# Performance work log

Measured on AMD Instinct MI355X. Metric: run time of the kernel, lower is better.

## Reference

```python
import jax, jax.numpy as jnp
import numpy as np

WS = 7       # window_size
NH = 4       # num_head = dim_in // dim_head
HD = 64      # dim_head
ALPHA = 0.1
BETA = 0.2
THETA = 0.5
EPS = 1e-5   # LayerNorm eps


def dwconv(x, w):
    # x: [b, C, h, w], w: [C, 1, k, k] depthwise, padding 'same', no bias
    return jax.lax.conv_general_dilated(
        x, w, window_strides=(1, 1), padding='SAME',
        feature_group_count=x.shape[1],
        dimension_numbers=('NCHW', 'OIHW', 'NCHW'))


def setup_inputs() -> dict:
    key = jax.random.key(0)
    ks = jax.random.split(key, 8)
    B, H, W, C = 32, 56, 56, 256
    s = 0.02
    return {
        'x': jax.random.normal(ks[0], (B, H, W, C), jnp.float32),
        'qkv_w': jax.random.normal(ks[1], (3 * C, C), jnp.float32) * s,
        'qkv_b': jnp.zeros((3 * C,), jnp.float32),
        'conv3_w': jax.random.normal(ks[2], (C, 1, 3, 3), jnp.float32) * s,
        'conv5_w': jax.random.normal(ks[3], (C, 1, 5, 5), jnp.float32) * s,
        'conv7_w': jax.random.normal(ks[4], (C, 1, 7, 7), jnp.float32) * s,
        'ffn_in_w': jax.random.normal(ks[5], (C, C), jnp.float32) * s,
        'ffn_out_w': jax.random.normal(ks[6], (C, C), jnp.float32) * s,
        'ln_g': jnp.ones((C,), jnp.float32),
        'ln_b': jnp.zeros((C,), jnp.float32),
    }


def reference(x, qkv_w, qkv_b, conv3_w, conv5_w, conv7_w, ffn_in_w, ffn_out_w, ln_g, ln_b):
    B, H, W, C = x.shape
    n1, n2 = H // WS, W // WS  # H,W divisible by WS -> no padding path
    # rearrange 'b (h1 n1) (w1 n2) c -> (b n1 n2) h1 w1 c' (window dim is MAJOR axis)
    xw = x.reshape(B, WS, n1, WS, n2, C).transpose(0, 2, 4, 1, 3, 5)
    xw = xw.reshape(B * n1 * n2, WS, WS, C)
    b, hw = B * n1 * n2, WS * WS

    shortcut = xw.reshape(b, hw, NH, HD).transpose(0, 2, 1, 3)  # [b, nh, hw, hd]
    qkv = xw.reshape(b, hw, C) @ qkv_w.T + qkv_b                # [b, hw, 3C]
    qkv = qkv.reshape(b, hw, 3, NH, HD).transpose(2, 0, 3, 1, 4)
    q, k, v = qkv[0], qkv[1], qkv[2]
    v = ALPHA * v + shortcut                                     # scaled residual into V
    shortcut2 = v.transpose(0, 2, 1, 3).reshape(b, WS, WS, C)    # [b, h, w, C]

    # SDPA with default scale hd^-0.5
    attn = jax.nn.softmax(jnp.einsum('bnqd,bnkd->bnqk', q, k) * (HD ** -0.5), axis=-1)
    x_spa = jnp.einsum('bnqk,bnkd->bnqd', attn, v)
    x_spa = x_spa.transpose(0, 2, 1, 3).reshape(b, WS, WS, C)

    # conv branches on modified v: v.transpose(-1,-2).reshape(b, C, h, w)
    xc = v.transpose(0, 1, 3, 2).reshape(b, C, WS, WS)
    c3 = dwconv(xc, conv3_w).transpose(0, 2, 3, 1)
    c5 = dwconv(xc, conv5_w).transpose(0, 2, 3, 1)
    c7 = dwconv(xc, conv7_w).transpose(0, 2, 3, 1)
    x_spa = 0.25 * (x_spa + c3 + c5 + c7)  # equal 0.25 branch weights

    xw = BETA * x_spa + shortcut2
    # inverse rearrange '(b n1 n2) h1 w1 c -> b (h1 n1) (w1 n2) c'
    xo = xw.reshape(B, n1, n2, WS, WS, C).transpose(0, 3, 1, 4, 2, 5).reshape(B, H, W, C)

    # FFN (bias=False) with scaled residual, then LayerNorm
    y = jax.nn.silu(xo @ ffn_in_w.T) @ ffn_out_w.T
    xo = THETA * y + xo
    mu = jnp.mean(xo, axis=-1, keepdims=True)
    var = jnp.var(xo, axis=-1, keepdims=True)
    return (xo - mu) / jnp.sqrt(var + EPS) * ln_g + ln_b
```

## Files before the change

kernel.cpp:

```cpp
#include <hip/hip_runtime.h>

typedef unsigned short u16;
typedef unsigned short u16x8 __attribute__((ext_vector_type(8)));
typedef unsigned short u16x4 __attribute__((ext_vector_type(4)));
typedef unsigned int   u32x2 __attribute__((ext_vector_type(2)));
typedef short          s16x8 __attribute__((ext_vector_type(8)));
typedef float          f32x4 __attribute__((ext_vector_type(4)));

#define DEV static __device__ __forceinline__

DEV float bf2f(u16 u){ unsigned int v = ((unsigned int)u) << 16; return __builtin_bit_cast(float, v); }
DEV u16 f2bf(float f){
  unsigned int u = __builtin_bit_cast(unsigned int, f);
  u += 0x7fffu + ((u >> 16) & 1u);
  return (u16)(u >> 16);
}

DEV f32x4 mfma16(u16x8 a, u16x8 b, f32x4 c){
  return __builtin_amdgcn_mfma_f32_16x16x32_bf16(
      __builtin_bit_cast(s16x8, a), __builtin_bit_cast(s16x8, b), c, 0, 0, 0);
}

DEV void g2l16(const void* g, void* l){
  __builtin_amdgcn_global_load_lds((const __attribute__((address_space(1))) void*)g,
                                   (__attribute__((address_space(3))) void*)l, 16, 0, 0);
}

DEV size_t xrow_from(int b, int hw){
  int h1 = hw / 7, w1 = hw - h1 * 7;
  return ((size_t)(((b >> 6) * 56 + h1 * 8 + ((b >> 3) & 7)) * 56 + (w1 * 8 + (b & 7)))) << 8;
}
DEV size_t xrow_off(int t){ int b = t / 49; return xrow_from(b, t - b * 49); }

__global__ __launch_bounds__(256) void k_prep(const float* __restrict__ qkvw,
                                              const float* __restrict__ c3,
                                              const float* __restrict__ c5,
                                              const float* __restrict__ c7,
                                              const float* __restrict__ fin,
                                              const float* __restrict__ fout,
                                              u16* __restrict__ wq, u16* __restrict__ wfi,
                                              u16* __restrict__ wfo, float* __restrict__ weff){
  int id = blockIdx.x * 256 + threadIdx.x;
  if (id < 196608) { wq[id] = f2bf(qkvw[id]); return; }
  id -= 196608;
  if (id < 65536) { wfi[id] = f2bf(fin[id]); return; }
  id -= 65536;
  if (id < 65536) { wfo[id] = f2bf(fout[id]); return; }
  id -= 65536;
  if (id < 12544) {
    int c = id / 49, t = id - c * 49;
    int di = t / 7 - 3, dj = t % 7 - 3;
    float s = c7[c * 49 + t];
    if (di >= -2 && di <= 2 && dj >= -2 && dj <= 2) s += c5[c * 25 + (di + 2) * 5 + (dj + 2)];
    if (di >= -1 && di <= 1 && dj >= -1 && dj <= 1) s += c3[c * 9 + (di + 1) * 3 + (dj + 1)];
    weff[t * 256 + c] = 0.05f * s;
  }
}

__global__ __launch_bounds__(256) void k_xbf(const float* __restrict__ x, u16* __restrict__ xbf){
  int tid = threadIdx.x;
  int tok = blockIdx.x * 4 + (tid >> 6);
  int c4 = (tid & 63) * 4;
  float4 v = *(const float4*)(x + xrow_off(tok) + c4);
  u16x4 o; o[0] = f2bf(v.x); o[1] = f2bf(v.y); o[2] = f2bf(v.z); o[3] = f2bf(v.w);
  *(u16x4*)&xbf[(size_t)tok * 256 + c4] = o;
}

__global__ __launch_bounds__(256) void k_qkv(const u16* __restrict__ xbf,
                                             const u16* __restrict__ wq,
                                             const float* __restrict__ qkvb,
                                             u16* __restrict__ qb, u16* __restrict__ kb,
                                             u16* __restrict__ vmb){
  __shared__ __align__(16) u16 As[128 * 64];
  __shared__ __align__(16) u16 Bs[128 * 64];
  const int bid = blockIdx.x;
  const int lin = (bid & 7) * 588 + (bid >> 3);
  const int bm = lin / 6, bn = lin - bm * 6;
  const int tid = threadIdx.x, lane = tid & 63, wid = tid >> 6;
  const int wm = wid >> 1, wn = wid & 1;
  const int r = lane & 15, g = lane >> 4;
  const int lr = lane >> 3;
  const int swz = ((lane & 7) ^ lr) * 16;
  const f32x4 fz = {0.f, 0.f, 0.f, 0.f};
  f32x4 acc[4][4];
#pragma unroll
  for (int m = 0; m < 4; ++m)
#pragma unroll
    for (int n = 0; n < 4; ++n) acc[m][n] = fz;

  const char* gA0 = (const char*)xbf + (size_t)bm * 128 * 512;
  const char* gB0 = (const char*)wq  + (size_t)bn * 128 * 512;

  for (int kt = 0; kt < 4; ++kt) {
#pragma unroll
    for (int ri = 0; ri < 4; ++ri) {
      int chunk = ri * 4 + wid;
      int row = chunk * 8 + lr;
      g2l16(gA0 + (size_t)row * 512 + kt * 128 + swz, (char*)As + chunk * 1024);
      g2l16(gB0 + (size_t)row * 512 + kt * 128 + swz, (char*)Bs + chunk * 1024);
    }
    __syncthreads();
#pragma unroll
    for (int kk = 0; kk < 2; ++kk) {
      u16x8 af[4], bq[4];
#pragma unroll
      for (int m = 0; m < 4; ++m)
        af[m] = *(const u16x8*)&As[(wm * 64 + m * 16 + r) * 64 + (((kk * 4 + g) ^ (r & 7)) * 8)];
#pragma unroll
      for (int n = 0; n < 4; ++n)
        bq[n] = *(const u16x8*)&Bs[(wn * 64 + n * 16 + r) * 64 + (((kk * 4 + g) ^ (r & 7)) * 8)];
#pragma unroll
      for (int m = 0; m < 4; ++m)
#pragma unroll
        for (int n = 0; n < 4; ++n) acc[m][n] = mfma16(af[m], bq[n], acc[m][n]);
    }
    __syncthreads();
  }

  const int sec = bn >> 1;
  const int colbase = bn * 128 + wn * 64;
  float bias[4];
#pragma unroll
  for (int n = 0; n < 4; ++n) bias[n] = qkvb[colbase + n * 16 + r];
#pragma unroll
  for (int m = 0; m < 4; ++m) {
#pragma unroll
    for (int i = 0; i < 4; ++i) {
      int t = bm * 128 + wm * 64 + m * 16 + g * 4 + i;
      int b = t / 49, hw = t - b * 49;
      size_t tokbase = (size_t)b * 12544;
#pragma unroll
      for (int n = 0; n < 4; ++n) {
        int col = colbase + n * 16 + r;
        float v = acc[m][n][i] + bias[n];
        if (sec == 0) {
          int c = col;
          qb[tokbase + (size_t)(c >> 6) * 3136 + hw * 64 + (c & 63)] = f2bf(v * 0.125f);
        } else if (sec == 1) {
          int c = col - 256;
          kb[tokbase + (size_t)(c >> 6) * 3136 + hw * 64 + (c & 63)] = f2bf(v);
        } else {
          int c = col - 512;
          float xv = bf2f(xbf[(size_t)t * 256 + c]);
          vmb[tokbase + (size_t)(c >> 6) * 3136 + hw * 64 + (c & 63)] = f2bf(0.1f * v + xv);
        }
      }
    }
  }
}

template<int HW0, int NPIX>
DEV void conv_do(const float (&in_f)[49], const float (&wreg)[49], const u16* xs,
                 int c, size_t obase, u16* __restrict__ xo){
#pragma unroll
  for (int p = 0; p < NPIX; ++p) {
    const int hw = HW0 + p;
    const int i0 = hw / 7, j0 = hw % 7;
    float a = 0.f;
#pragma unroll
    for (int di = -3; di <= 3; ++di) {
      const int ii = i0 + di;
      if (ii < 0 || ii > 6) continue;
#pragma unroll
      for (int dj = -3; dj <= 3; ++dj) {
        const int jj = j0 + dj;
        if (jj < 0 || jj > 6) continue;
        a += in_f[ii * 7 + jj] * wreg[(di + 3) * 7 + (dj + 3)];
      }
    }
    float xsv = bf2f(xs[hw * 72 + c]);
    float outv = in_f[hw] + 0.05f * xsv + a;
    xo[obase + (size_t)hw * 128] = f2bf(outv);
  }
}

__global__ __launch_bounds__(256) void k_attn(const u16* __restrict__ qb,
                                              const u16* __restrict__ kb,
                                              const u16* __restrict__ vmb,
                                              const float* __restrict__ weff,
                                              u16* __restrict__ xo){
  __shared__ __align__(16) u16 smem[2 * 16272];
  const int bx = blockIdx.x;
  const int b = bx >> 1, hp = bx & 1;
  const int tid = threadIdx.x, lane = tid & 63, wid = tid >> 6;
  const int hl = wid >> 1, hf = wid & 1;
  const int hg = hp * 2 + hl;
  const int base = hl * 16272;
  const int qo = base, ko = base + 3528, vto = base + 7056, po = base + 11664;
  const int r = lane & 15, g = lane >> 4;
  const size_t hbase = (size_t)(b * 4 + hg) * 3136;

  if (hf == 1) {
#pragma unroll
    for (int rr = 0; rr < 7; ++rr) {
      int ci = rr * 64 + lane;
      if (ci < 392) {
        int hw = ci >> 3, c16 = ci & 7;
        *(u16x8*)&smem[qo + hw * 72 + c16 * 8] = *(const u16x8*)&qb[hbase + hw * 64 + c16 * 8];
      }
    }
#pragma unroll
    for (int rr = 0; rr < 7; ++rr) {
      int ci = rr * 64 + lane;
      if (ci < 392) {
        int hw = ci >> 3, c16 = ci & 7;
        *(u16x8*)&smem[ko + hw * 72 + c16 * 8] = *(const u16x8*)&kb[hbase + hw * 64 + c16 * 8];
      }
    }
  } else {
    int c = lane;
    u16 pix[49];
#pragma unroll
    for (int hw = 0; hw < 49; ++hw) pix[hw] = vmb[hbase + hw * 64 + c];
#pragma unroll
    for (int t2 = 0; t2 < 12; ++t2) {
      u32x2 w;
      w[0] = (unsigned)pix[4 * t2] | ((unsigned)pix[4 * t2 + 1] << 16);
      w[1] = (unsigned)pix[4 * t2 + 2] | ((unsigned)pix[4 * t2 + 3] << 16);
      *(u32x2*)&smem[vto + c * 72 + 4 * t2] = w;
    }
    u32x2 wl; wl[0] = (unsigned)pix[48]; wl[1] = 0u;
    *(u32x2*)&smem[vto + c * 72 + 48] = wl;
    u32x2 z; z[0] = 0u; z[1] = 0u;
    *(u32x2*)&smem[vto + c * 72 + 52] = z;
    *(u32x2*)&smem[vto + c * 72 + 56] = z;
    *(u32x2*)&smem[vto + c * 72 + 60] = z;
  }
  __syncthreads();

  const int mt0 = hf * 2;
  const f32x4 fz = {0.f, 0.f, 0.f, 0.f};
  f32x4 s[2][4];
#pragma unroll
  for (int m = 0; m < 2; ++m)
#pragma unroll
    for (int n = 0; n < 4; ++n) s[m][n] = fz;
#pragma unroll
  for (int kk = 0; kk < 2; ++kk) {
    u16x8 aq[2], bk[4];
#pragma unroll
    for (int m = 0; m < 2; ++m) aq[m] = *(const u16x8*)&smem[qo + ((mt0 + m) * 16 + r) * 72 + kk * 32 + g * 8];
#pragma unroll
    for (int n = 0; n < 4; ++n) bk[n] = *(const u16x8*)&smem[ko + (n * 16 + r) * 72 + kk * 32 + g * 8];
#pragma unroll
    for (int m = 0; m < 2; ++m)
#pragma unroll
      for (int n = 0; n < 4; ++n) s[m][n] = mfma16(aq[m], bk[n], s[m][n]);
  }

#pragma unroll
  for (int m = 0; m < 2; ++m) {
#pragma unroll
    for (int i = 0; i < 4; ++i) {
      float x0 = s[m][0][i], x1 = s[m][1][i], x2 = s[m][2][i];
      float x3 = (r >= 1) ? -1e30f : s[m][3][i];
      float mx = fmaxf(fmaxf(x0, x1), fmaxf(x2, x3));
#pragma unroll
      for (int off = 1; off < 16; off <<= 1) mx = fmaxf(mx, __shfl_xor(mx, off, 64));
      float e0 = __expf(x0 - mx), e1 = __expf(x1 - mx), e2 = __expf(x2 - mx);
      float e3 = (r >= 1) ? 0.f : __expf(x3 - mx);
      float sum = e0 + e1 + e2 + e3;
#pragma unroll
      for (int off = 1; off < 16; off <<= 1) sum += __shfl_xor(sum, off, 64);
      float inv = 1.f / sum;
      int rowp = po + ((mt0 + m) * 16 + g * 4 + i) * 72;
      smem[rowp + r]       = f2bf(e0 * inv);
      smem[rowp + 16 + r]  = f2bf(e1 * inv);
      smem[rowp + 32 + r]  = f2bf(e2 * inv);
      smem[rowp + 48 + r]  = f2bf(e3 * inv);
    }
  }

  f32x4 o[2][4];
#pragma unroll
  for (int m = 0; m < 2; ++m)
#pragma unroll
    for (int n = 0; n < 4; ++n) o[m][n] = fz;
#pragma unroll
  for (int kk = 0; kk < 2; ++kk) {
    u16x8 pa[2], vb[4];
#pragma unroll
    for (int m = 0; m < 2; ++m) pa[m] = *(const u16x8*)&smem[po + ((mt0 + m) * 16 + r) * 72 + kk * 32 + g * 8];
#pragma unroll
    for (int n = 0; n < 4; ++n) vb[n] = *(const u16x8*)&smem[vto + (n * 16 + r) * 72 + kk * 32 + g * 8];
#pragma unroll
    for (int m = 0; m < 2; ++m)
#pragma unroll
      for (int n = 0; n < 4; ++n) o[m][n] = mfma16(pa[m], vb[n], o[m][n]);
  }
#pragma unroll
  for (int m = 0; m < 2; ++m)
#pragma unroll
    for (int n = 0; n < 4; ++n)
#pragma unroll
      for (int i = 0; i < 4; ++i)
        smem[po + ((mt0 + m) * 16 + g * 4 + i) * 72 + n * 16 + r] = f2bf(o[m][n][i]);
  __syncthreads();

  {
    int c = lane;
    float in_f[49];
#pragma unroll
    for (int t2 = 0; t2 < 6; ++t2) {
      u16x8 raw = *(const u16x8*)&smem[vto + c * 72 + t2 * 8];
#pragma unroll
      for (int e = 0; e < 8; ++e) in_f[t2 * 8 + e] = bf2f(raw[e]);
    }
    in_f[48] = bf2f(smem[vto + c * 72 + 48]);
    float wreg[49];
#pragma unroll
    for (int t2 = 0; t2 < 49; ++t2) wreg[t2] = weff[t2 * 256 + hg * 64 + c];
    size_t obase = (size_t)b * 12544 + (size_t)hp * 6272 + (size_t)(hl * 64 + c);
    if (hf == 0) conv_do<0, 25>(in_f, wreg, &smem[po], c, obase, xo);
    else         conv_do<25, 24>(in_f, wreg, &smem[po], c, obase, xo);
  }
}

__global__ __launch_bounds__(256) void k_ffn1(const u16* __restrict__ xo,
                                              const u16* __restrict__ wfi,
                                              u16* __restrict__ h){
  __shared__ __align__(16) u16 As[128 * 64];
  __shared__ __align__(16) u16 Bs[128 * 64];
  const int bid = blockIdx.x;
  const int lin = (bid & 7) * 196 + (bid >> 3);
  const int bm = lin >> 1, bn = lin & 1;
  const int tid = threadIdx.x, lane = tid & 63, wid = tid >> 6;
  const int wm = wid >> 1, wn = wid & 1;
  const int r = lane & 15, g = lane >> 4;
  const int lr = lane >> 3;
  const int swz = ((lane & 7) ^ lr) * 16;
  const f32x4 fz = {0.f, 0.f, 0.f, 0.f};
  f32x4 acc[4][4];
#pragma unroll
  for (int m = 0; m < 4; ++m)
#pragma unroll
    for (int n = 0; n < 4; ++n) acc[m][n] = fz;

  for (int kt = 0; kt < 4; ++kt) {
#pragma unroll
    for (int ri = 0; ri < 4; ++ri) {
      int chunk = ri * 4 + wid;
      int row = chunk * 8 + lr;
      int t = bm * 128 + row;
      int b49 = t / 49, hw = t - b49 * 49;
      size_t off = (size_t)b49 * 12544 + (size_t)(kt >> 1) * 6272 + (size_t)hw * 128 + (kt & 1) * 64;
      g2l16((const char*)xo + off * 2 + swz, (char*)As + chunk * 1024);
      g2l16((const char*)wfi + (size_t)(bn * 128 + row) * 512 + kt * 128 + swz, (char*)Bs + chunk * 1024);
    }
    __syncthreads();
#pragma unroll
    for (int kk = 0; kk < 2; ++kk) {
      u16x8 af[4], bq[4];
#pragma unroll
      for (int m = 0; m < 4; ++m)
        af[m] = *(const u16x8*)&As[(wm * 64 + m * 16 + r) * 64 + (((kk * 4 + g) ^ (r & 7)) * 8)];
#pragma unroll
      for (int n = 0; n < 4; ++n)
        bq[n] = *(const u16x8*)&Bs[(wn * 64 + n * 16 + r) * 64 + (((kk * 4 + g) ^ (r & 7)) * 8)];
#pragma unroll
      for (int m = 0; m < 4; ++m)
#pragma unroll
        for (int n = 0; n < 4; ++n) acc[m][n] = mfma16(af[m], bq[n], acc[m][n]);
    }
    __syncthreads();
  }
#pragma unroll
  for (int m = 0; m < 4; ++m)
#pragma unroll
    for (int i = 0; i < 4; ++i) {
      int t = bm * 128 + wm * 64 + m * 16 + g * 4 + i;
#pragma unroll
      for (int n = 0; n < 4; ++n) {
        int col = bn * 128 + wn * 64 + n * 16 + r;
        float v = acc[m][n][i];
        float sg = v / (1.f + __expf(-v));
        h[(size_t)t * 256 + col] = f2bf(sg);
      }
    }
}

__global__ __launch_bounds__(512) void k_ffn2(const u16* __restrict__ h,
                                              const u16* __restrict__ wfo,
                                              const u16* __restrict__ xo,
                                              const float* __restrict__ lng,
                                              const float* __restrict__ lnb,
                                              float* __restrict__ out){
  __shared__ __align__(16) u16 As[128 * 64];
  __shared__ __align__(16) u16 Bs[256 * 64];
  __shared__ float red1[4][128];
  __shared__ float red2[4][128];
  const int bm = blockIdx.x;
  const int tid = threadIdx.x, lane = tid & 63, wid = tid >> 6;
  const int wm = wid >> 2, wn = wid & 3;
  const int r = lane & 15, g = lane >> 4;
  const int lr = lane >> 3;
  const int swz = ((lane & 7) ^ lr) * 16;
  const f32x4 fz = {0.f, 0.f, 0.f, 0.f};
  f32x4 acc[4][4];
#pragma unroll
  for (int m = 0; m < 4; ++m)
#pragma unroll
    for (int n = 0; n < 4; ++n) acc[m][n] = fz;

  for (int kt = 0; kt < 4; ++kt) {
#pragma unroll
    for (int ri = 0; ri < 2; ++ri) {
      int chunk = ri * 8 + wid;
      int row = chunk * 8 + lr;
      g2l16((const char*)h + (size_t)(bm * 128 + row) * 512 + kt * 128 + swz, (char*)As + chunk * 1024);
    }
#pragma unroll
    for (int ri = 0; ri < 4; ++ri) {
      int chunk = ri * 8 + wid;
      int row = chunk * 8 + lr;
      g2l16((const char*)wfo + (size_t)row * 512 + kt * 128 + swz, (char*)Bs + chunk * 1024);
    }
    __syncthreads();
#pragma unroll
    for (int kk = 0; kk < 2; ++kk) {
      u16x8 af[4], bq[4];
#pragma unroll
      for (int m = 0; m < 4; ++m)
        af[m] = *(const u16x8*)&As[(wm * 64 + m * 16 + r) * 64 + (((kk * 4 + g) ^ (r & 7)) * 8)];
#pragma unroll
      for (int n = 0; n < 4; ++n)
        bq[n] = *(const u16x8*)&Bs[(wn * 64 + n * 16 + r) * 64 + (((kk * 4 + g) ^ (r & 7)) * 8)];
#pragma unroll
      for (int m = 0; m < 4; ++m)
#pragma unroll
        for (int n = 0; n < 4; ++n) acc[m][n] = mfma16(af[m], bq[n], acc[m][n]);
    }
    __syncthreads();
  }

  float lg[4], lb[4];
#pragma unroll
  for (int n = 0; n < 4; ++n) {
    int col = wn * 64 + n * 16 + r;
    lg[n] = lng[col]; lb[n] = lnb[col];
  }
#pragma unroll
  for (int m = 0; m < 4; ++m)
#pragma unroll
    for (int i = 0; i < 4; ++i) {
      int t = bm * 128 + wm * 64 + m * 16 + g * 4 + i;
      int b49 = t / 49, hw = t - b49 * 49;
      size_t xbase = (size_t)b49 * 12544 + (size_t)hw * 128;
#pragma unroll
      for (int n = 0; n < 4; ++n) {
        int col = wn * 64 + n * 16 + r;
        acc[m][n][i] = 0.5f * acc[m][n][i] + bf2f(xo[xbase + (col >> 7) * 6272 + (col & 127)]);
      }
    }
#pragma unroll
  for (int m = 0; m < 4; ++m)
#pragma unroll
    for (int i = 0; i < 4; ++i) {
      float s1 = 0.f, s2 = 0.f;
#pragma unroll
      for (int n = 0; n < 4; ++n) { float v = acc[m][n][i]; s1 += v; s2 += v * v; }
#pragma unroll
      for (int off = 1; off < 16; off <<= 1) { s1 += __shfl_xor(s1, off, 64); s2 += __shfl_xor(s2, off, 64); }
      if (r == 0) {
        int rl = wm * 64 + m * 16 + g * 4 + i;
        red1[wn][rl] = s1; red2[wn][rl] = s2;
      }
    }
  __syncthreads();
#pragma unroll
  for (int m = 0; m < 4; ++m)
#pragma unroll
    for (int i = 0; i < 4; ++i) {
      int rl = wm * 64 + m * 16 + g * 4 + i;
      float S1 = red1[0][rl] + red1[1][rl] + red1[2][rl] + red1[3][rl];
      float S2 = red2[0][rl] + red2[1][rl] + red2[2][rl] + red2[3][rl];
      float mu = S1 * (1.f / 256.f);
      float var = S2 * (1.f / 256.f) - mu * mu;
      float rstd = rsqrtf(var + 1e-5f);
      int t = bm * 128 + rl;
      int b49 = t / 49, hw = t - b49 * 49;
      size_t ob = xrow_from(b49, hw);
#pragma unroll
      for (int n = 0; n < 4; ++n) {
        int col = wn * 64 + n * 16 + r;
        out[ob + col] = (acc[m][n][i] - mu) * rstd * lg[n] + lb[n];
      }
    }
}

extern "C" void kernel_launch(void* const* d_in, const int* in_sizes, int n_in,
                              void* d_out, int out_size, void* d_ws, size_t ws_size,
                              hipStream_t stream) {
  (void)in_sizes; (void)n_in; (void)out_size; (void)ws_size;
  const float* x     = (const float*)d_in[0];
  const float* qkvw  = (const float*)d_in[1];
  const float* qkvb  = (const float*)d_in[2];
  const float* c3    = (const float*)d_in[3];
  const float* c5    = (const float*)d_in[4];
  const float* c7    = (const float*)d_in[5];
  const float* fin   = (const float*)d_in[6];
  const float* fout  = (const float*)d_in[7];
  const float* lng   = (const float*)d_in[8];
  const float* lnb   = (const float*)d_in[9];
  float* out = (float*)d_out;
  char* ws = (char*)d_ws;

  u16*   qbuf = (u16*)(ws);
  u16*   kbuf = (u16*)(ws + 51380224);
  u16*   vmb  = (u16*)(ws + 102760448);
  u16*   wq   = (u16*)(ws + 154140672);
  u16*   wfi  = (u16*)(ws + 154533888);
  u16*   wfo  = (u16*)(ws + 154664960);
  float* weff = (float*)(ws + 154796032);
  u16*   xbf  = (u16*)d_out;

  k_prep<<<dim3(1329), dim3(256), 0, stream>>>(qkvw, c3, c5, c7, fin, fout, wq, wfi, wfo, weff);
  k_xbf<<<dim3(25088), dim3(256), 0, stream>>>(x, xbf);
  k_qkv<<<dim3(4704), dim3(256), 0, stream>>>(xbf, wq, qkvb, qbuf, kbuf, vmb);
  k_attn<<<dim3(4096), dim3(256), 0, stream>>>(qbuf, kbuf, vmb, weff, kbuf );
  k_ffn1<<<dim3(1568), dim3(256), 0, stream>>>(kbuf , wfi, qbuf );
  k_ffn2<<<dim3(784), dim3(512), 0, stream>>>(qbuf , wfo, kbuf , lng, lnb, out);
}
```

Before: 310.7 us.

## Fuse input conversion, QKV projection, attention and conv into one per-window kernel

Replaces the separate bf16 conversion, QKV GEMM and attention kernels with a single kernel that handles one 7x7 window per block. Each block loads and converts x into LDS, computes Q, K and V(mod) with MFMA, reading the weights straight from global memory, then runs softmax attention and the combined depthwise conv, all in LDS. This removes the global round trips for xbf, q, k and v and two kernel launches. In exchange it uses a large LDS footprint (about 132 KB), pads each window's 49 tokens to 64, and every block reloads the full QKV weight from global or cache, which may limit occupancy.

```diff
diff --git a/kernel.cpp b/kernel.cpp
--- a/kernel.cpp
+++ b/kernel.cpp
@@ -3,7 +3,6 @@
 typedef unsigned short u16;
 typedef unsigned short u16x8 __attribute__((ext_vector_type(8)));
 typedef unsigned short u16x4 __attribute__((ext_vector_type(4)));
-typedef unsigned int   u32x2 __attribute__((ext_vector_type(2)));
 typedef short          s16x8 __attribute__((ext_vector_type(8)));
 typedef float          f32x4 __attribute__((ext_vector_type(4)));
 
@@ -25,12 +24,6 @@
   __builtin_amdgcn_global_load_lds((const __attribute__((address_space(1))) void*)g,
                                    (__attribute__((address_space(3))) void*)l, 16, 0, 0);
 }
-
-DEV size_t xrow_from(int b, int hw){
-  int h1 = hw / 7, w1 = hw - h1 * 7;
-  return ((size_t)(((b >> 6) * 56 + h1 * 8 + ((b >> 3) & 7)) * 56 + (w1 * 8 + (b & 7)))) << 8;
-}
-DEV size_t xrow_off(int t){ int b = t / 49; return xrow_from(b, t - b * 49); }
 
 __global__ __launch_bounds__(256) void k_prep(const float* __restrict__ qkvw,
                                               const float* __restrict__ c3,
@@ -57,199 +50,116 @@
   }
 }
 
-__global__ __launch_bounds__(256) void k_xbf(const float* __restrict__ x, u16* __restrict__ xbf){
-  int tid = threadIdx.x;
-  int tok = blockIdx.x * 4 + (tid >> 6);
-  int c4 = (tid & 63) * 4;
-  float4 v = *(const float4*)(x + xrow_off(tok) + c4);
-  u16x4 o; o[0] = f2bf(v.x); o[1] = f2bf(v.y); o[2] = f2bf(v.z); o[3] = f2bf(v.w);
-  *(u16x4*)&xbf[(size_t)tok * 256 + c4] = o;
-}
-
-__global__ __launch_bounds__(256) void k_qkv(const u16* __restrict__ xbf,
+__global__ __launch_bounds__(256) void k_fqa(const float* __restrict__ x,
                                              const u16* __restrict__ wq,
                                              const float* __restrict__ qkvb,
-                                             u16* __restrict__ qb, u16* __restrict__ kb,
-                                             u16* __restrict__ vmb){
-  __shared__ __align__(16) u16 As[128 * 64];
-  __shared__ __align__(16) u16 Bs[128 * 64];
-  const int bid = blockIdx.x;
-  const int lin = (bid & 7) * 588 + (bid >> 3);
-  const int bm = lin / 6, bn = lin - bm * 6;
-  const int tid = threadIdx.x, lane = tid & 63, wid = tid >> 6;
-  const int wm = wid >> 1, wn = wid & 1;
+                                             const float* __restrict__ weff,
+                                             u16* __restrict__ xo){
+  __shared__ __align__(16) u16 smem[67584];
+  const int win = blockIdx.x;
+  const int tid = threadIdx.x, lane = tid & 63, w = tid >> 6;
   const int r = lane & 15, g = lane >> 4;
-  const int lr = lane >> 3;
-  const int swz = ((lane & 7) ^ lr) * 16;
+  const int b32 = win >> 6, n1 = (win >> 3) & 7, n2 = win & 7;
+  const int QO = 16384, KO = 32768, VO = 49152;
   const f32x4 fz = {0.f, 0.f, 0.f, 0.f};
-  f32x4 acc[4][4];
-#pragma unroll
-  for (int m = 0; m < 4; ++m)
-#pragma unroll
-    for (int n = 0; n < 4; ++n) acc[m][n] = fz;
-
-  const char* gA0 = (const char*)xbf + (size_t)bm * 128 * 512;
-  const char* gB0 = (const char*)wq  + (size_t)bn * 128 * 512;
-
-  for (int kt = 0; kt < 4; ++kt) {
-#pragma unroll
-    for (int ri = 0; ri < 4; ++ri) {
-      int chunk = ri * 4 + wid;
-      int row = chunk * 8 + lr;
-      g2l16(gA0 + (size_t)row * 512 + kt * 128 + swz, (char*)As + chunk * 1024);
-      g2l16(gB0 + (size_t)row * 512 + kt * 128 + swz, (char*)Bs + chunk * 1024);
-    }
-    __syncthreads();
-#pragma unroll
-    for (int kk = 0; kk < 2; ++kk) {
+
+  {
+    int row = tid >> 2, seg = tid & 3;
+    if (row < 49) {
+      int h1 = row / 7, w1 = row - h1 * 7;
+      const float* src = x + ((size_t)((b32 * 56 + h1 * 8 + n1) * 56 + w1 * 8 + n2) << 8);
+#pragma unroll
+      for (int j = 0; j < 8; ++j) {
+        int blk = seg * 8 + j;
+        float4 v0 = *(const float4*)(src + blk * 8);
+        float4 v1 = *(const float4*)(src + blk * 8 + 4);
+        u16x8 o;
+        o[0] = f2bf(v0.x); o[1] = f2bf(v0.y); o[2] = f2bf(v0.z); o[3] = f2bf(v0.w);
+        o[4] = f2bf(v1.x); o[5] = f2bf(v1.y); o[6] = f2bf(v1.z); o[7] = f2bf(v1.w);
+        *(u16x8*)&smem[row * 256 + (blk ^ (row & 7)) * 8] = o;
+      }
+    } else {
+      u16x8 z = {0, 0, 0, 0, 0, 0, 0, 0};
+#pragma unroll
+      for (int j = 0; j < 8; ++j) {
+        int blk = seg * 8 + j;
+        *(u16x8*)&smem[row * 256 + (blk ^ (row & 7)) * 8] = z;
+      }
+    }
+  }
+  __syncthreads();
+
+#pragma unroll
+  for (int p = 0; p < 3; ++p) {
+    const int wcol = p * 256 + w * 64;
+    float bias[4];
+#pragma unroll
+    for (int n = 0; n < 4; ++n) bias[n] = qkvb[wcol + n * 16 + r];
+    f32x4 acc[4][4];
+#pragma unroll
+    for (int m = 0; m < 4; ++m)
+#pragma unroll
+      for (int n = 0; n < 4; ++n) acc[m][n] = fz;
+
+#pragma unroll
+    for (int kk = 0; kk < 8; ++kk) {
       u16x8 af[4], bq[4];
 #pragma unroll
       for (int m = 0; m < 4; ++m)
-        af[m] = *(const u16x8*)&As[(wm * 64 + m * 16 + r) * 64 + (((kk * 4 + g) ^ (r & 7)) * 8)];
+        af[m] = *(const u16x8*)&smem[(m * 16 + r) * 256 + (((kk * 4 + g) ^ (r & 7)) * 8)];
 #pragma unroll
       for (int n = 0; n < 4; ++n)
-        bq[n] = *(const u16x8*)&Bs[(wn * 64 + n * 16 + r) * 64 + (((kk * 4 + g) ^ (r & 7)) * 8)];
+        bq[n] = *(const u16x8*)&wq[(size_t)(wcol + n * 16 + r) * 256 + kk * 32 + g * 8];
 #pragma unroll
       for (int m = 0; m < 4; ++m)
 #pragma unroll
         for (int n = 0; n < 4; ++n) acc[m][n] = mfma16(af[m], bq[n], acc[m][n]);
     }
-    __syncthreads();
-  }
-
-  const int sec = bn >> 1;
-  const int colbase = bn * 128 + wn * 64;
-  float bias[4];
-#pragma unroll
-  for (int n = 0; n < 4; ++n) bias[n] = qkvb[colbase + n * 16 + r];
+#pragma unroll
+    for (int m = 0; m < 4; ++m)
+#pragma unroll
+      for (int i = 0; i < 4; ++i) {
+        int t = m * 16 + 4 * g + i;
+#pragma unroll
+        for (int n = 0; n < 4; ++n) {
+          int d = n * 16 + r;
+          float v = acc[m][n][i] + bias[n];
+          if (p == 0) {
+            smem[QO + w * 4096 + t * 64 + (((d >> 3) ^ (t & 7)) * 8) + (d & 7)] = f2bf(v * 0.125f);
+          } else if (p == 1) {
+            smem[KO + w * 4096 + t * 64 + (((d >> 3) ^ (t & 7)) * 8) + (d & 7)] = f2bf(v);
+          } else {
+            int ch = w * 64 + d;
+            float xv = bf2f(smem[t * 256 + (((ch >> 3) ^ (t & 7)) * 8) + (ch & 7)]);
+            smem[VO + w * 4608 + d * 72 + t] = f2bf(0.1f * v + xv);
+          }
+        }
+      }
+  }
+  __syncthreads();
+
+  f32x4 s[4][4];
+#pragma unroll
+  for (int m = 0; m < 4; ++m)
+#pragma unroll
+    for (int n = 0; n < 4; ++n) s[m][n] = fz;
+#pragma unroll
+  for (int kk = 0; kk < 2; ++kk) {
+    u16x8 aq[4], bk[4];
+#pragma unroll
+    for (int m = 0; m < 4; ++m)
+      aq[m] = *(const u16x8*)&smem[QO + w * 4096 + (m * 16 + r) * 64 + (((kk * 4 + g) ^ (r & 7)) * 8)];
+#pragma unroll
+    for (int n = 0; n < 4; ++n)
+      bk[n] = *(const u16x8*)&smem[KO + w * 4096 + (n * 16 + r) * 64 + (((kk * 4 + g) ^ (r & 7)) * 8)];
+#pragma unroll
+    for (int m = 0; m < 4; ++m)
+#pragma unroll
+      for (int n = 0; n < 4; ++n) s[m][n] = mfma16(aq[m], bk[n], s[m][n]);
+  }
+
 #pragma unroll
   for (int m = 0; m < 4; ++m) {
-#pragma unroll
-    for (int i = 0; i < 4; ++i) {
-      int t = bm * 128 + wm * 64 + m * 16 + g * 4 + i;
-      int b = t / 49, hw = t - b * 49;
-      size_t tokbase = (size_t)b * 12544;
-#pragma unroll
-      for (int n = 0; n < 4; ++n) {
-        int col = colbase + n * 16 + r;
-        float v = acc[m][n][i] + bias[n];
-        if (sec == 0) {
-          int c = col;
-          qb[tokbase + (size_t)(c >> 6) * 3136 + hw * 64 + (c & 63)] = f2bf(v * 0.125f);
-        } else if (sec == 1) {
-          int c = col - 256;
-          kb[tokbase + (size_t)(c >> 6) * 3136 + hw * 64 + (c & 63)] = f2bf(v);
-        } else {
-          int c = col - 512;
-          float xv = bf2f(xbf[(size_t)t * 256 + c]);
-          vmb[tokbase + (size_t)(c >> 6) * 3136 + hw * 64 + (c & 63)] = f2bf(0.1f * v + xv);
-        }
-      }
-    }
-  }
-}
-
-template<int HW0, int NPIX>
-DEV void conv_do(const float (&in_f)[49], const float (&wreg)[49], const u16* xs,
-                 int c, size_t obase, u16* __restrict__ xo){
-#pragma unroll
-  for (int p = 0; p < NPIX; ++p) {
-    const int hw = HW0 + p;
-    const int i0 = hw / 7, j0 = hw % 7;
-    float a = 0.f;
-#pragma unroll
-    for (int di = -3; di <= 3; ++di) {
-      const int ii = i0 + di;
-      if (ii < 0 || ii > 6) continue;
-#pragma unroll
-      for (int dj = -3; dj <= 3; ++dj) {
-        const int jj = j0 + dj;
-        if (jj < 0 || jj > 6) continue;
-        a += in_f[ii * 7 + jj] * wreg[(di + 3) * 7 + (dj + 3)];
-      }
-    }
-    float xsv = bf2f(xs[hw * 72 + c]);
-    float outv = in_f[hw] + 0.05f * xsv + a;
-    xo[obase + (size_t)hw * 128] = f2bf(outv);
-  }
-}
-
-__global__ __launch_bounds__(256) void k_attn(const u16* __restrict__ qb,
-                                              const u16* __restrict__ kb,
-                                              const u16* __restrict__ vmb,
-                                              const float* __restrict__ weff,
-                                              u16* __restrict__ xo){
-  __shared__ __align__(16) u16 smem[2 * 16272];
-  const int bx = blockIdx.x;
-  const int b = bx >> 1, hp = bx & 1;
-  const int tid = threadIdx.x, lane = tid & 63, wid = tid >> 6;
-  const int hl = wid >> 1, hf = wid & 1;
-  const int hg = hp * 2 + hl;
-  const int base = hl * 16272;
-  const int qo = base, ko = base + 3528, vto = base + 7056, po = base + 11664;
-  const int r = lane & 15, g = lane >> 4;
-  const size_t hbase = (size_t)(b * 4 + hg) * 3136;
-
-  if (hf == 1) {
-#pragma unroll
-    for (int rr = 0; rr < 7; ++rr) {
-      int ci = rr * 64 + lane;
-      if (ci < 392) {
-        int hw = ci >> 3, c16 = ci & 7;
-        *(u16x8*)&smem[qo + hw * 72 + c16 * 8] = *(const u16x8*)&qb[hbase + hw * 64 + c16 * 8];
-      }
-    }
-#pragma unroll
-    for (int rr = 0; rr < 7; ++rr) {
-      int ci = rr * 64 + lane;
-      if (ci < 392) {
-        int hw = ci >> 3, c16 = ci & 7;
-        *(u16x8*)&smem[ko + hw * 72 + c16 * 8] = *(const u16x8*)&kb[hbase + hw * 64 + c16 * 8];
-      }
-    }
-  } else {
-    int c = lane;
-    u16 pix[49];
-#pragma unroll
-    for (int hw = 0; hw < 49; ++hw) pix[hw] = vmb[hbase + hw * 64 + c];
-#pragma unroll
-    for (int t2 = 0; t2 < 12; ++t2) {
-      u32x2 w;
-      w[0] = (unsigned)pix[4 * t2] | ((unsigned)pix[4 * t2 + 1] << 16);
-      w[1] = (unsigned)pix[4 * t2 + 2] | ((unsigned)pix[4 * t2 + 3] << 16);
-      *(u32x2*)&smem[vto + c * 72 + 4 * t2] = w;
-    }
-    u32x2 wl; wl[0] = (unsigned)pix[48]; wl[1] = 0u;
-    *(u32x2*)&smem[vto + c * 72 + 48] = wl;
-    u32x2 z; z[0] = 0u; z[1] = 0u;
-    *(u32x2*)&smem[vto + c * 72 + 52] = z;
-    *(u32x2*)&smem[vto + c * 72 + 56] = z;
-    *(u32x2*)&smem[vto + c * 72 + 60] = z;
-  }
-  __syncthreads();
-
-  const int mt0 = hf * 2;
-  const f32x4 fz = {0.f, 0.f, 0.f, 0.f};
-  f32x4 s[2][4];
-#pragma unroll
-  for (int m = 0; m < 2; ++m)
-#pragma unroll
-    for (int n = 0; n < 4; ++n) s[m][n] = fz;
-#pragma unroll
-  for (int kk = 0; kk < 2; ++kk) {
-    u16x8 aq[2], bk[4];
-#pragma unroll
-    for (int m = 0; m < 2; ++m) aq[m] = *(const u16x8*)&smem[qo + ((mt0 + m) * 16 + r) * 72 + kk * 32 + g * 8];
-#pragma unroll
-    for (int n = 0; n < 4; ++n) bk[n] = *(const u16x8*)&smem[ko + (n * 16 + r) * 72 + kk * 32 + g * 8];
-#pragma unroll
-    for (int m = 0; m < 2; ++m)
-#pragma unroll
-      for (int n = 0; n < 4; ++n) s[m][n] = mfma16(aq[m], bk[n], s[m][n]);
-  }
-
-#pragma unroll
-  for (int m = 0; m < 2; ++m) {
 #pragma unroll
     for (int i = 0; i < 4; ++i) {
       float x0 = s[m][0][i], x1 = s[m][1][i], x2 = s[m][2][i];
@@ -263,56 +173,79 @@
 #pragma unroll
       for (int off = 1; off < 16; off <<= 1) sum += __shfl_xor(sum, off, 64);
       float inv = 1.f / sum;
-      int rowp = po + ((mt0 + m) * 16 + g * 4 + i) * 72;
-      smem[rowp + r]       = f2bf(e0 * inv);
-      smem[rowp + 16 + r]  = f2bf(e1 * inv);
-      smem[rowp + 32 + r]  = f2bf(e2 * inv);
-      smem[rowp + 48 + r]  = f2bf(e3 * inv);
-    }
-  }
-
-  f32x4 o[2][4];
-#pragma unroll
-  for (int m = 0; m < 2; ++m)
-#pragma unroll
-    for (int n = 0; n < 4; ++n) o[m][n] = fz;
+      int q = m * 16 + 4 * g + i;
+      int base = w * 4096 + q * 64;
+      float ev[4] = {e0 * inv, e1 * inv, e2 * inv, e3 * inv};
+#pragma unroll
+      for (int n = 0; n < 4; ++n)
+        smem[base + (((n * 2 + (r >> 3)) ^ (q & 7)) * 8) + (r & 7)] = f2bf(ev[n]);
+    }
+  }
+
+  f32x4 o4[4][4];
+#pragma unroll
+  for (int m = 0; m < 4; ++m)
+#pragma unroll
+    for (int n = 0; n < 4; ++n) o4[m][n] = fz;
 #pragma unroll
   for (int kk = 0; kk < 2; ++kk) {
-    u16x8 pa[2], vb[4];
-#pragma unroll
-    for (int m = 0; m < 2; ++m) pa[m] = *(const u16x8*)&smem[po + ((mt0 + m) * 16 + r) * 72 + kk * 32 + g * 8];
-#pragma unroll
-    for (int n = 0; n < 4; ++n) vb[n] = *(const u16x8*)&smem[vto + (n * 16 + r) * 72 + kk * 32 + g * 8];
-#pragma unroll
-    for (int m = 0; m < 2; ++m)
-#pragma unroll
-      for (int n = 0; n < 4; ++n) o[m][n] = mfma16(pa[m], vb[n], o[m][n]);
-  }
-#pragma unroll
-  for (int m = 0; m < 2; ++m)
+    u16x8 pa[4], bv[4];
+#pragma unroll
+    for (int m = 0; m < 4; ++m)
+      pa[m] = *(const u16x8*)&smem[w * 4096 + (m * 16 + r) * 64 + (((kk * 4 + g) ^ (r & 7)) * 8)];
 #pragma unroll
     for (int n = 0; n < 4; ++n)
-#pragma unroll
-      for (int i = 0; i < 4; ++i)
-        smem[po + ((mt0 + m) * 16 + g * 4 + i) * 72 + n * 16 + r] = f2bf(o[m][n][i]);
-  __syncthreads();
+      bv[n] = *(const u16x8*)&smem[VO + w * 4608 + (n * 16 + r) * 72 + kk * 32 + g * 8];
+#pragma unroll
+    for (int m = 0; m < 4; ++m)
+#pragma unroll
+      for (int n = 0; n < 4; ++n) o4[m][n] = mfma16(pa[m], bv[n], o4[m][n]);
+  }
+#pragma unroll
+  for (int m = 0; m < 4; ++m)
+#pragma unroll
+    for (int i = 0; i < 4; ++i) {
+      int q = m * 16 + 4 * g + i;
+      int base = w * 4096 + q * 64;
+#pragma unroll
+      for (int n = 0; n < 4; ++n) {
+        int d = n * 16 + r;
+        smem[base + (((d >> 3) ^ (q & 7)) * 8) + (d & 7)] = f2bf(o4[m][n][i]);
+      }
+    }
 
   {
-    int c = lane;
+    const int c = lane;
     float in_f[49];
 #pragma unroll
     for (int t2 = 0; t2 < 6; ++t2) {
-      u16x8 raw = *(const u16x8*)&smem[vto + c * 72 + t2 * 8];
+      u16x8 raw = *(const u16x8*)&smem[VO + w * 4608 + c * 72 + t2 * 8];
 #pragma unroll
       for (int e = 0; e < 8; ++e) in_f[t2 * 8 + e] = bf2f(raw[e]);
     }
-    in_f[48] = bf2f(smem[vto + c * 72 + 48]);
+    in_f[48] = bf2f(smem[VO + w * 4608 + c * 72 + 48]);
     float wreg[49];
 #pragma unroll
-    for (int t2 = 0; t2 < 49; ++t2) wreg[t2] = weff[t2 * 256 + hg * 64 + c];
-    size_t obase = (size_t)b * 12544 + (size_t)hp * 6272 + (size_t)(hl * 64 + c);
-    if (hf == 0) conv_do<0, 25>(in_f, wreg, &smem[po], c, obase, xo);
-    else         conv_do<25, 24>(in_f, wreg, &smem[po], c, obase, xo);
+    for (int t2 = 0; t2 < 49; ++t2) wreg[t2] = weff[t2 * 256 + w * 64 + c];
+    u16* xob = xo + (size_t)win * 12544 + (size_t)w * 3136 + c;
+#pragma unroll
+    for (int hw = 0; hw < 49; ++hw) {
+      const int i0 = hw / 7, j0 = hw % 7;
+      float a = 0.f;
+#pragma unroll
+      for (int di = -3; di <= 3; ++di) {
+        const int ii = i0 + di;
+        if (ii < 0 || ii > 6) continue;
+#pragma unroll
+        for (int dj = -3; dj <= 3; ++dj) {
+          const int jj = j0 + dj;
+          if (jj < 0 || jj > 6) continue;
+          a += in_f[ii * 7 + jj] * wreg[(di + 3) * 7 + (dj + 3)];
+        }
+      }
+      float xsv = bf2f(smem[w * 4096 + hw * 64 + (((c >> 3) ^ (hw & 7)) * 8) + (c & 7)]);
+      xob[(size_t)hw * 64] = f2bf(in_f[hw] + 0.05f * xsv + a);
+    }
   }
 }
 
@@ -342,8 +275,8 @@
       int chunk = ri * 4 + wid;
       int row = chunk * 8 + lr;
       int t = bm * 128 + row;
-      int b49 = t / 49, hw = t - b49 * 49;
-      size_t off = (size_t)b49 * 12544 + (size_t)(kt >> 1) * 6272 + (size_t)hw * 128 + (kt & 1) * 64;
+      int win = t / 49, hw = t - win * 49;
+      size_t off = (size_t)win * 12544 + (size_t)kt * 3136 + (size_t)hw * 64;
       g2l16((const char*)xo + off * 2 + swz, (char*)As + chunk * 1024);
       g2l16((const char*)wfi + (size_t)(bn * 128 + row) * 512 + kt * 128 + swz, (char*)Bs + chunk * 1024);
     }
@@ -377,6 +310,11 @@
         h[(size_t)t * 256 + col] = f2bf(sg);
       }
     }
+}
+
+DEV size_t xrow_from(int b, int hw){
+  int h1 = hw / 7, w1 = hw - h1 * 7;
+  return ((size_t)(((b >> 6) * 56 + h1 * 8 + ((b >> 3) & 7)) * 56 + (w1 * 8 + (b & 7)))) << 8;
 }
 
 __global__ __launch_bounds__(512) void k_ffn2(const u16* __restrict__ h,
@@ -445,11 +383,11 @@
     for (int i = 0; i < 4; ++i) {
       int t = bm * 128 + wm * 64 + m * 16 + g * 4 + i;
       int b49 = t / 49, hw = t - b49 * 49;
-      size_t xbase = (size_t)b49 * 12544 + (size_t)hw * 128;
+      size_t xbase = (size_t)b49 * 12544 + (size_t)hw * 64;
 #pragma unroll
       for (int n = 0; n < 4; ++n) {
         int col = wn * 64 + n * 16 + r;
-        acc[m][n][i] = 0.5f * acc[m][n][i] + bf2f(xo[xbase + (col >> 7) * 6272 + (col & 127)]);
+        acc[m][n][i] = 0.5f * acc[m][n][i] + bf2f(xo[xbase + (size_t)(col >> 6) * 3136 + (col & 63)]);
       }
     }
 #pragma unroll
@@ -505,19 +443,15 @@
   float* out = (float*)d_out;
   char* ws = (char*)d_ws;
 
-  u16*   qbuf = (u16*)(ws);
-  u16*   kbuf = (u16*)(ws + 51380224);
-  u16*   vmb  = (u16*)(ws + 102760448);
-  u16*   wq   = (u16*)(ws + 154140672);
-  u16*   wfi  = (u16*)(ws + 154533888);
-  u16*   wfo  = (u16*)(ws + 154664960);
-  float* weff = (float*)(ws + 154796032);
-  u16*   xbf  = (u16*)d_out;
+  u16*   xob  = (u16*)(ws);
+  u16*   hbuf = (u16*)(ws + 51380224);
+  u16*   wq   = (u16*)(ws + 102760448);
+  u16*   wfi  = (u16*)(ws + 103153664);
+  u16*   wfo  = (u16*)(ws + 103284736);
+  float* weff = (float*)(ws + 103415808);
 
   k_prep<<<dim3(1329), dim3(256), 0, stream>>>(qkvw, c3, c5, c7, fin, fout, wq, wfi, wfo, weff);
-  k_xbf<<<dim3(25088), dim3(256), 0, stream>>>(x, xbf);
-  k_qkv<<<dim3(4704), dim3(256), 0, stream>>>(xbf, wq, qkvb, qbuf, kbuf, vmb);
-  k_attn<<<dim3(4096), dim3(256), 0, stream>>>(qbuf, kbuf, vmb, weff, kbuf );
-  k_ffn1<<<dim3(1568), dim3(256), 0, stream>>>(kbuf , wfi, qbuf );
-  k_ffn2<<<dim3(784), dim3(512), 0, stream>>>(qbuf , wfo, kbuf , lng, lnb, out);
-}
+  k_fqa<<<dim3(2048), dim3(256), 0, stream>>>(x, wq, qkvb, weff, xob);
+  k_ffn1<<<dim3(1568), dim3(256), 0, stream>>>(xob, wfi, hbuf);
+  k_ffn2<<<dim3(784), dim3(512), 0, stream>>>(hbuf, wfo, xob, lng, lnb, out);
+}
```

Result: slower. 674.9 us (+117.2%).
